# Optimization experiments

Measured on AMD Instinct MI355X. Metric: run time of the kernel, lower is better.

## Reference

```python
import jax, jax.numpy as jnp
import numpy as np
from jax import lax

D_FEAT, SEQ_LEN, D_MODEL, N_HEAD, N_LAYERS, D_FF, BATCH = 20, 20, 512, 8, 3, 2048, 4096


def _pe(L, D):
    pos = jnp.arange(L, dtype=jnp.float32)[:, None]
    div = jnp.exp(jnp.arange(0, D, 2, dtype=jnp.float32) * (-np.log(10000.0) / D))
    pe = jnp.zeros((L, D), dtype=jnp.float32)
    pe = pe.at[:, 0::2].set(jnp.sin(pos * div)).at[:, 1::2].set(jnp.cos(pos * div))
    return pe


def _ln(x, g, b, eps=1e-5):
    m = x.mean(-1, keepdims=True)
    v = ((x - m) ** 2).mean(-1, keepdims=True)
    return (x - m) * lax.rsqrt(v + eps) * g + b


def _circ_conv(x, w):
    # x [B,C,L]: Conv1d(C->1, k=3, circular padding=1, no bias) -> [B,L]
    xs = jnp.stack([jnp.roll(x, 1, -1), x, jnp.roll(x, -1, -1)], -1)  # [B,C,L,3]
    return jnp.einsum('bclk,ck->bl', xs, w)


def _projector(x, stats, wconv, W0, b0, W1, b1, W2):
    y = _circ_conv(x, wconv)                       # [B, d_feat]
    z = jnp.concatenate([y, stats[:, 0, :]], -1)   # [B, 2*d_feat]
    h = jax.nn.relu(z @ W0.T + b0)
    h = jax.nn.relu(h @ W1.T + b1)
    return h @ W2.T                                # no bias on last layer


def setup_inputs():
    key = jax.random.key(0)
    ks = iter(jax.random.split(key, 64))
    nrm = lambda shape, s=0.02: jax.random.normal(next(ks), shape, dtype=jnp.float32) * s
    zeros = lambda shape: jnp.zeros(shape, jnp.float32)
    ones = lambda shape: jnp.ones(shape, jnp.float32)
    return {
        'src': jax.random.normal(next(ks), (BATCH, SEQ_LEN, D_FEAT), dtype=jnp.float32),
        'W_feat': nrm((D_MODEL, D_FEAT)), 'b_feat': zeros((D_MODEL,)),
        'tau_conv': nrm((SEQ_LEN, 3), 0.1),
        'tau_W0': nrm((D_MODEL, 2 * D_FEAT)), 'tau_b0': zeros((D_MODEL,)),
        'tau_W1': nrm((D_MODEL, D_MODEL)), 'tau_b1': zeros((D_MODEL,)),
        'tau_W2': nrm((1, D_MODEL)),
        'del_conv': nrm((SEQ_LEN, 3), 0.1),
        'del_W0': nrm((D_MODEL, 2 * D_FEAT)), 'del_b0': zeros((D_MODEL,)),
        'del_W1': nrm((D_MODEL, D_MODEL)), 'del_b1': zeros((D_MODEL,)),
        'del_W2': nrm((SEQ_LEN, D_MODEL)),
        'Wq': nrm((N_LAYERS, D_MODEL, D_MODEL)), 'bq': zeros((N_LAYERS, D_MODEL)),
        'Wk': nrm((N_LAYERS, D_MODEL, D_MODEL)), 'bk': zeros((N_LAYERS, D_MODEL)),
        'Wv': nrm((N_LAYERS, D_MODEL, D_MODEL)), 'bv': zeros((N_LAYERS, D_MODEL)),
        'Wo': nrm((N_LAYERS, D_MODEL, D_MODEL)), 'bo': zeros((N_LAYERS, D_MODEL)),
        'Wc1': nrm((N_LAYERS, D_FF, D_MODEL)), 'bc1': zeros((N_LAYERS, D_FF)),
        'Wc2': nrm((N_LAYERS, D_MODEL, D_FF)), 'bc2': zeros((N_LAYERS, D_MODEL)),
        'ln1_g': ones((N_LAYERS, D_MODEL)), 'ln1_b': zeros((N_LAYERS, D_MODEL)),
        'ln2_g': ones((N_LAYERS, D_MODEL)), 'ln2_b': zeros((N_LAYERS, D_MODEL)),
        'lnf_g': ones((D_MODEL,)), 'lnf_b': zeros((D_MODEL,)),
        'W_pre': nrm((SEQ_LEN, D_MODEL)), 'b_pre': zeros((SEQ_LEN,)),
        'W_dec': nrm((1, SEQ_LEN)), 'b_dec': zeros((1,)),
    }


def reference(src, W_feat, b_feat, tau_conv, tau_W0, tau_b0, tau_W1, tau_b1, tau_W2,
              del_conv, del_W0, del_b0, del_W1, del_b1, del_W2,
              Wq, bq, Wk, bk, Wv, bv, Wo, bo, Wc1, bc1, Wc2, bc2,
              ln1_g, ln1_b, ln2_g, ln2_b, lnf_g, lnf_b, W_pre, b_pre, W_dec, b_dec):
    B, L, F = src.shape
    H = N_HEAD
    x_raw = lax.stop_gradient(src)
    mean_src = lax.stop_gradient(jnp.mean(src, axis=1, keepdims=True))        # [B,1,F]
    s = src - mean_src
    std_src = lax.stop_gradient(jnp.sqrt(jnp.var(s, axis=1, keepdims=True) + 1e-5))
    s = s / std_src
    tau = jnp.exp(_projector(x_raw, std_src, tau_conv, tau_W0, tau_b0, tau_W1, tau_b1, tau_W2))  # [B,1]
    delta = _projector(x_raw, mean_src, del_conv, del_W0, del_b0, del_W1, del_b1, del_W2)        # [B,L]
    x = s @ W_feat.T + b_feat + _pe(L, W_feat.shape[0])[None]                 # [B,L,D]
    dh = x.shape[-1] // H
    scale = np.float32(1.0 / np.sqrt(dh))
    for i in range(Wq.shape[0]):
        q = (x @ Wq[i].T + bq[i]).reshape(B, L, H, dh)
        k = (x @ Wk[i].T + bk[i]).reshape(B, L, H, dh)
        v = (x @ Wv[i].T + bv[i]).reshape(B, L, H, dh)
        # DSAttention: tau-rescaled, delta-shifted scores
        scores = jnp.einsum('blhe,bshe->bhls', q, k) * tau[:, :, None, None] + delta[:, None, None, :]
        A = jax.nn.softmax(scale * scores, axis=-1)
        o = jnp.einsum('bhls,bshd->blhd', A, v).reshape(B, L, -1)
        x = x + (o @ Wo[i].T + bo[i])
        x = _ln(x, ln1_g[i], ln1_b[i])
        y = jax.nn.relu(x @ Wc1[i].T + bc1[i])        # conv1d k=1 == linear
        y = y @ Wc2[i].T + bc2[i]
        x = _ln(x + y, ln2_g[i], ln2_b[i])
    x = _ln(x, lnf_g, lnf_b)
    out = (x @ W_pre.T + b_pre) * std_src + mean_src  # [B,L,L] (d_feat == seq_len)
    out = out[:, -1, :] @ W_dec.T + b_dec             # [B,1]
    return out[:, 0]
```

## Files before the change

### kernel.cpp

```cpp
#include <hip/hip_runtime.h>
#include <math.h>
#include <stdint.h>

#define BB 4096
#define LL 20
#define FE 20
#define DD 512
#define HH 8
#define DHD 64
#define FFD 2048
#define NLAY 3

typedef __bf16 bf16x8 __attribute__((ext_vector_type(8)));
typedef float f32x4 __attribute__((ext_vector_type(4)));

__device__ __forceinline__ void gload_lds16(const unsigned short* g, unsigned short* l){
  __builtin_amdgcn_global_load_lds(
      (const __attribute__((address_space(1))) void*)g,
      (__attribute__((address_space(3))) void*)l, 16, 0, 0);
}

__device__ __forceinline__ float wsum(float v){
#pragma unroll
  for (int o = 32; o > 0; o >>= 1) v += __shfl_xor(v, o, 64);
  return v;
}

__device__ __forceinline__ unsigned short f2b(float f){
  unsigned u = __float_as_uint(f);
  u += 0x7FFFu + ((u >> 16) & 1u);
  return (unsigned short)(u >> 16);
}
__device__ __forceinline__ float b2f(unsigned short b){
  return __uint_as_float(((unsigned)b) << 16);
}

__device__ __forceinline__ int2 xcd_swz(){
  const int nx = gridDim.x;
  const int nwg = nx * gridDim.y;
  const int orig = blockIdx.y * nx + blockIdx.x;
  const int q = nwg >> 3, r = nwg & 7;
  const int xcd = orig & 7, idx = orig >> 3;
  const int wg = (xcd < r ? xcd*(q+1) : r*(q+1) + (xcd-r)*q) + idx;
  return make_int2(wg % nx, wg / nx);
}

template<bool RELU, bool BIAS, bool RES>
__global__ __launch_bounds__(256) void bgemm(
    const unsigned short* __restrict__ A, int lda,
    const unsigned short* __restrict__ W, int ldw,
    const float* __restrict__ bias,
    const unsigned short* res, int ldr,
    unsigned short* __restrict__ Cout, int ldc, int K)
{
  __shared__ __align__(16) unsigned short Asm[2][128*32];
  __shared__ __align__(16) unsigned short Bsm[2][128*32];
  const int2 swz = xcd_swz();
  const int bn = swz.x << 7, bm = swz.y << 7;
  const int tid = threadIdx.x;
  const int wave = tid >> 6, lane = tid & 63;
  const int wr = wave >> 1, wc = wave & 1;
  const int sr = lane >> 2, slot = lane & 3;
  const int rg = lane & 15, cg = lane >> 4;

  f32x4 acc[4][4];
#pragma unroll
  for (int i = 0; i < 4; ++i)
#pragma unroll
    for (int j = 0; j < 4; ++j) acc[i][j] = (f32x4){0.f,0.f,0.f,0.f};

  auto stage = [&](int kt, int b){
    const int k0 = kt << 5;
#pragma unroll
    for (int i = 0; i < 2; ++i) {
      const int r  = (i<<6) + (wave<<4) + sr;
      const int ch = slot ^ ((r>>1)&3);
      gload_lds16(A + (size_t)(bm + r)*lda + k0 + (ch<<3),
                  &Asm[b][((i<<6) + (wave<<4))*32]);
      gload_lds16(W + (size_t)(bn + r)*ldw + k0 + (ch<<3),
                  &Bsm[b][((i<<6) + (wave<<4))*32]);
    }
  };

  auto compute = [&](int b){
    bf16x8 af[4], bfr[4];
#pragma unroll
    for (int mi = 0; mi < 4; ++mi){
      int r = (wr<<6) + (mi<<4) + rg;
      af[mi] = *(const bf16x8*)&Asm[b][r*32 + ((cg ^ ((r>>1)&3))<<3)];
    }
#pragma unroll
    for (int ni = 0; ni < 4; ++ni){
      int r = (wc<<6) + (ni<<4) + rg;
      bfr[ni] = *(const bf16x8*)&Bsm[b][r*32 + ((cg ^ ((r>>1)&3))<<3)];
    }
#pragma unroll
    for (int mi = 0; mi < 4; ++mi)
#pragma unroll
      for (int ni = 0; ni < 4; ++ni)
        acc[mi][ni] = __builtin_amdgcn_mfma_f32_16x16x32_bf16(af[mi], bfr[ni], acc[mi][ni], 0, 0, 0);
  };

  const int nt = K >> 5;
  stage(0, 0);
  __syncthreads();
  int cur = 0;
  for (int t = 0; t < nt; ++t){
    if (t + 1 < nt) stage(t + 1, cur ^ 1);
    compute(cur);
    __syncthreads();
    cur ^= 1;
  }

#pragma unroll
  for (int mi = 0; mi < 4; ++mi){
#pragma unroll
    for (int ni = 0; ni < 4; ++ni){
      const int row0 = bm + (wr<<6) + (mi<<4) + (cg<<2);
      const int col  = bn + (wc<<6) + (ni<<4) + rg;
      float bv = BIAS ? bias[col] : 0.f;
#pragma unroll
      for (int j = 0; j < 4; ++j){
        float v = acc[mi][ni][j] + bv;
        if (RES)  v += b2f(res[(size_t)(row0+j)*ldr + col]);
        if (RELU) v = fmaxf(v, 0.f);
        Cout[(size_t)(row0+j)*ldc + col] = f2b(v);
      }
    }
  }
}

template<bool RELU, bool BIAS, bool RES>
__global__ __launch_bounds__(256) void bgemm64(
    const unsigned short* __restrict__ A, int lda,
    const unsigned short* __restrict__ W, int ldw,
    const float* __restrict__ bias,
    const unsigned short* res, int ldr,
    unsigned short* __restrict__ Cout, int ldc, int K)
{
  __shared__ __align__(16) unsigned short Asm[2][64*32];
  __shared__ __align__(16) unsigned short Bsm[2][128*32];
  const int2 swz = xcd_swz();
  const int bn = swz.x << 7, bm = swz.y << 6;
  const int tid = threadIdx.x;
  const int wave = tid >> 6, lane = tid & 63;
  const int sr = lane >> 2, slot = lane & 3;
  const int rg = lane & 15, cg = lane >> 4;

  f32x4 acc[4][2];
#pragma unroll
  for (int i = 0; i < 4; ++i)
#pragma unroll
    for (int j = 0; j < 2; ++j) acc[i][j] = (f32x4){0.f,0.f,0.f,0.f};

  auto stage = [&](int kt, int b){
    const int k0 = kt << 5;
    {
      const int r  = (wave<<4) + sr;
      const int ch = slot ^ ((r>>1)&3);
      gload_lds16(A + (size_t)(bm + r)*lda + k0 + (ch<<3),
                  &Asm[b][(wave<<4)*32]);
    }
#pragma unroll
    for (int i = 0; i < 2; ++i) {
      const int r  = (i<<6) + (wave<<4) + sr;
      const int ch = slot ^ ((r>>1)&3);
      gload_lds16(W + (size_t)(bn + r)*ldw + k0 + (ch<<3),
                  &Bsm[b][((i<<6) + (wave<<4))*32]);
    }
  };

  auto compute = [&](int b){
    bf16x8 af[4], bfr[2];
#pragma unroll
    for (int mi = 0; mi < 4; ++mi){
      int r = (mi<<4) + rg;
      af[mi] = *(const bf16x8*)&Asm[b][r*32 + ((cg ^ ((r>>1)&3))<<3)];
    }
#pragma unroll
    for (int ni = 0; ni < 2; ++ni){
      int r = (wave<<5) + (ni<<4) + rg;
      bfr[ni] = *(const bf16x8*)&Bsm[b][r*32 + ((cg ^ ((r>>1)&3))<<3)];
    }
#pragma unroll
    for (int mi = 0; mi < 4; ++mi)
#pragma unroll
      for (int ni = 0; ni < 2; ++ni)
        acc[mi][ni] = __builtin_amdgcn_mfma_f32_16x16x32_bf16(af[mi], bfr[ni], acc[mi][ni], 0, 0, 0);
  };

  const int nt = K >> 5;
  stage(0, 0);
  __syncthreads();
  int cur = 0;
  for (int t = 0; t < nt; ++t){
    if (t + 1 < nt) stage(t + 1, cur ^ 1);
    compute(cur);
    __syncthreads();
    cur ^= 1;
  }

#pragma unroll
  for (int mi = 0; mi < 4; ++mi){
#pragma unroll
    for (int ni = 0; ni < 2; ++ni){
      const int row0 = bm + (mi<<4) + (cg<<2);
      const int col  = bn + (wave<<5) + (ni<<4) + rg;
      float bv = BIAS ? bias[col] : 0.f;
#pragma unroll
      for (int j = 0; j < 4; ++j){
        float v = acc[mi][ni][j] + bv;
        if (RES)  v += b2f(res[(size_t)(row0+j)*ldr + col]);
        if (RELU) v = fmaxf(v, 0.f);
        Cout[(size_t)(row0+j)*ldc + col] = f2b(v);
      }
    }
  }
}

template<bool RELU, bool BIAS, bool PE>
__global__ __launch_bounds__(256) void gemm_xwt(
    const float* __restrict__ A, int lda,
    const float* __restrict__ W, int ldw,
    const float* __restrict__ bias,
    float* __restrict__ C, int ldc,
    int M, int N, int K,
    const float* __restrict__ pe, unsigned short* __restrict__ xbout)
{
  __shared__ float As[16][72];
  __shared__ float Ws[16][72];
  const int bm = blockIdx.y << 6, bn = blockIdx.x << 6;
  const int tid = threadIdx.x;
  const int tx = tid & 15, ty = tid >> 4;
  const int lr = tid >> 2;
  const int lc = (tid & 3) << 2;
  float acc[4][4] = {{0.f}};
  const float* Ap = A + (size_t)(bm + lr) * lda;
  const float* Wp = W + (size_t)(bn + lr) * ldw;
  for (int k0 = 0; k0 < K; k0 += 16) {
    float4 av, wv;
    if (k0 + 16 <= K) {
      av = *(const float4*)(Ap + k0 + lc);
      wv = *(const float4*)(Wp + k0 + lc);
    } else {
      float aa[4] = {0,0,0,0}, ww[4] = {0,0,0,0};
#pragma unroll
      for (int j = 0; j < 4; ++j){ int kk = k0 + lc + j; if (kk < K){ aa[j] = Ap[kk]; ww[j] = Wp[kk]; } }
      av = make_float4(aa[0],aa[1],aa[2],aa[3]);
      wv = make_float4(ww[0],ww[1],ww[2],ww[3]);
    }
    As[lc+0][lr]=av.x; As[lc+1][lr]=av.y; As[lc+2][lr]=av.z; As[lc+3][lr]=av.w;
    Ws[lc+0][lr]=wv.x; Ws[lc+1][lr]=wv.y; Ws[lc+2][lr]=wv.z; Ws[lc+3][lr]=wv.w;
    __syncthreads();
#pragma unroll
    for (int k = 0; k < 16; ++k) {
      const float4 a = *(const float4*)(&As[k][ty<<2]);
      const float4 b = *(const float4*)(&Ws[k][tx<<2]);
      acc[0][0]+=a.x*b.x; acc[0][1]+=a.x*b.y; acc[0][2]+=a.x*b.z; acc[0][3]+=a.x*b.w;
      acc[1][0]+=a.y*b.x; acc[1][1]+=a.y*b.y; acc[1][2]+=a.y*b.z; acc[1][3]+=a.y*b.w;
      acc[2][0]+=a.z*b.x; acc[2][1]+=a.z*b.y; acc[2][2]+=a.z*b.z; acc[2][3]+=a.z*b.w;
      acc[3][0]+=a.w*b.x; acc[3][1]+=a.w*b.y; acc[3][2]+=a.w*b.z; acc[3][3]+=a.w*b.w;
    }
    __syncthreads();
  }
#pragma unroll
  for (int i = 0; i < 4; ++i) {
    const int m = bm + (ty<<2) + i;
#pragma unroll
    for (int j = 0; j < 4; ++j) {
      const int col = bn + (tx<<2) + j;
      float v = acc[i][j];
      if (BIAS) v += bias[col];
      if (PE)   v += pe[(m % LL)*DD + col];
      if (RELU) v = fmaxf(v, 0.f);
      if (PE) xbout[(size_t)m*ldc + col] = f2b(v);
      else    C[(size_t)m*ldc + col] = v;
    }
  }
}

__global__ void cvt_bf16_kernel(const float* __restrict__ in, unsigned short* __restrict__ out, int n){
  int i = blockIdx.x * 256 + threadIdx.x;
  if (i < n) out[i] = f2b(in[i]);
}

__global__ void concat_bias_kernel(const float* __restrict__ bq, const float* __restrict__ bk,
                                   const float* __restrict__ bv, float* __restrict__ bqkv){
  int i = blockIdx.x * 256 + threadIdx.x;
  if (i >= NLAY*1536) return;
  int l = i / 1536, r = i % 1536;
  int s = r >> 9, j = r & 511;
  const float* srcp = (s == 0) ? bq : (s == 1) ? bk : bv;
  bqkv[i] = srcp[l*DD + j];
}

__global__ void pe_kernel(float* __restrict__ pe){
  int i = blockIdx.x * 256 + threadIdx.x;
  int l = i >> 8, hd = i & 255;
  float dv = expf((2.f * hd) * (-9.210340371976184f / 512.f));
  float a = (float)l * dv;
  pe[l*DD + 2*hd]     = sinf(a);
  pe[l*DD + 2*hd + 1] = cosf(a);
}

__global__ void stats_kernel(const float* __restrict__ src, float* __restrict__ mean,
                             float* __restrict__ stdv, int nbf){
  int i = blockIdx.x * 256 + threadIdx.x;
  if (i >= nbf) return;
  int b = i / FE, f = i % FE;
  const float* p = src + (size_t)b * (LL*FE) + f;
  float v[LL]; float s = 0.f;
#pragma unroll
  for (int l = 0; l < LL; ++l){ v[l] = p[l*FE]; s += v[l]; }
  float m = s * (1.f/LL);
  float q = 0.f;
#pragma unroll
  for (int l = 0; l < LL; ++l){ float d = v[l]-m; q += d*d; }
  mean[i] = m;
  stdv[i] = sqrtf(q * (1.f/LL) + 1e-5f);
}

__global__ void snorm_kernel(const float* __restrict__ src, const float* __restrict__ mean,
                             const float* __restrict__ stdv, float* __restrict__ s, int n){
  int i = blockIdx.x * 256 + threadIdx.x;
  if (i >= n) return;
  int b = i / (LL*FE);
  int f = i % FE;
  int bf = b*FE + f;
  s[i] = (src[i] - mean[bf]) / stdv[bf];
}

__global__ __launch_bounds__(64) void convz_kernel(
    const float* __restrict__ src, const float* __restrict__ wt, const float* __restrict__ wd,
    const float* __restrict__ mean, const float* __restrict__ stdv,
    float* __restrict__ z_tau, float* __restrict__ z_del)
{
  int b = blockIdx.x;
  __shared__ float ss[LL*FE];
  __shared__ float wct[LL*3], wcd[LL*3];
  for (int idx = threadIdx.x; idx < LL*FE; idx += 64) ss[idx] = src[(size_t)b*LL*FE + idx];
  if (threadIdx.x < 60){ wct[threadIdx.x] = wt[threadIdx.x]; wcd[threadIdx.x] = wd[threadIdx.x]; }
  __syncthreads();
  if (threadIdx.x < 40) {
    int f = threadIdx.x % FE;
    bool isdel = threadIdx.x >= FE;
    const float* w = isdel ? wcd : wct;
    int fm = (f + FE - 1) % FE, fp = (f + 1) % FE;
    float acc = 0.f;
#pragma unroll
    for (int t = 0; t < LL; ++t){
      const float* r = ss + t*FE;
      acc += r[fm]*w[t*3+0] + r[f]*w[t*3+1] + r[fp]*w[t*3+2];
    }
    if (isdel){ z_del[b*40 + f] = acc; z_del[b*40 + 20 + f] = mean[b*FE + f]; }
    else      { z_tau[b*40 + f] = acc; z_tau[b*40 + 20 + f] = stdv[b*FE + f]; }
  }
}

__global__ __launch_bounds__(256) void tau_head(const float* __restrict__ h, const float* __restrict__ W2, float* __restrict__ tau){
  const int b = (blockIdx.x << 2) + (threadIdx.x >> 6);
  const int lane = threadIdx.x & 63;
  const float* hb = h + (size_t)b * DD;
  float s = 0.f;
#pragma unroll
  for (int j = 0; j < 8; ++j){ int d0 = lane + j*64; s += hb[d0]*W2[d0]; }
  s = wsum(s);
  if (lane == 0) tau[b] = expf(s);
}

__global__ __launch_bounds__(256) void delta_head(const float* __restrict__ h, const float* __restrict__ W2, float* __restrict__ delta){
  const int b = blockIdx.x;
  const int w = threadIdx.x >> 6, lane = threadIdx.x & 63;
  const float* hb = h + (size_t)b * DD;
  for (int f = w; f < FE; f += 4){
    float s = 0.f;
#pragma unroll
    for (int j = 0; j < 8; ++j){ int d0 = lane + j*64; s += hb[d0]*W2[(size_t)f*DD + d0]; }
    s = wsum(s);
    if (lane == 0) delta[b*FE + f] = s;
  }
}

__global__ __launch_bounds__(256) void attn_kernel(
    unsigned short* __restrict__ qkv,
    const float* __restrict__ tau, const float* __restrict__ delta)
{
  const int bh = blockIdx.x;
  const int b = bh >> 3, h = bh & 7;
  __shared__ float qs[LL][68];
  __shared__ float kt[DHD][25];
  __shared__ float vs[LL][DHD];
  __shared__ float ps[LL][LL+1];
  const size_t base = (size_t)b * LL * 1536 + h * DHD;
  unsigned short* qg = qkv + base;
  const unsigned short* kg = qkv + base + 512;
  const unsigned short* vg = qkv + base + 1024;

  for (int it = threadIdx.x; it < LL*16; it += 256) {
    const int l = it >> 4, c = it & 15;
    const ushort4 qv = *(const ushort4*)(qg + l*1536 + c*4);
    const ushort4 kv = *(const ushort4*)(kg + l*1536 + c*4);
    const ushort4 vv = *(const ushort4*)(vg + l*1536 + c*4);
    qs[l][c*4+0]=b2f(qv.x); qs[l][c*4+1]=b2f(qv.y); qs[l][c*4+2]=b2f(qv.z); qs[l][c*4+3]=b2f(qv.w);
    kt[c*4+0][l]=b2f(kv.x); kt[c*4+1][l]=b2f(kv.y); kt[c*4+2][l]=b2f(kv.z); kt[c*4+3][l]=b2f(kv.w);
    vs[l][c*4+0]=b2f(vv.x); vs[l][c*4+1]=b2f(vv.y); vs[l][c*4+2]=b2f(vv.z); vs[l][c*4+3]=b2f(vv.w);
  }
  __syncthreads();

  const float ta = tau[b];
  for (int idx = threadIdx.x; idx < LL*LL; idx += 256) {
    const int l = idx / LL, s2 = idx % LL;
    float d = 0.f;
#pragma unroll
    for (int e = 0; e < DHD; ++e) d += qs[l][e]*kt[e][s2];
    ps[l][s2] = 0.125f * (d * ta + delta[b*FE + s2]);
  }
  __syncthreads();

  if (threadIdx.x < LL) {
    const int l = threadIdx.x;
    float m = -1e30f;
#pragma unroll
    for (int s2 = 0; s2 < LL; ++s2) m = fmaxf(m, ps[l][s2]);
    float sum = 0.f;
#pragma unroll
    for (int s2 = 0; s2 < LL; ++s2){ float e2 = expf(ps[l][s2]-m); ps[l][s2] = e2; sum += e2; }
    const float r = 1.f / sum;
#pragma unroll
    for (int s2 = 0; s2 < LL; ++s2) ps[l][s2] *= r;
  }
  __syncthreads();

  for (int it = threadIdx.x; it < LL*16; it += 256) {
    const int l = it >> 4, c = it & 15;
    float4 o = {0.f,0.f,0.f,0.f};
#pragma unroll
    for (int s2 = 0; s2 < LL; ++s2) {
      const float p = ps[l][s2];
      const float4 vv = *(const float4*)&vs[s2][c*4];
      o.x += p*vv.x; o.y += p*vv.y; o.z += p*vv.z; o.w += p*vv.w;
    }
    ushort4 ov;
    ov.x = f2b(o.x); ov.y = f2b(o.y); ov.z = f2b(o.z); ov.w = f2b(o.w);
    *(ushort4*)(qg + l*1536 + c*4) = ov;
  }
}

__global__ __launch_bounds__(64) void attn19_kernel(
    const unsigned short* __restrict__ kvb, const unsigned short* __restrict__ q19,
    unsigned short* __restrict__ o19,
    const float* __restrict__ tau, const float* __restrict__ delta)
{
  const int bh = blockIdx.x;
  const int b = bh >> 3, h = bh & 7;
  __shared__ float ks[LL][DHD], vs[LL][DHD];
  const unsigned short* kg = kvb + (size_t)b * LL * 1024 + h * DHD;
  const unsigned short* vg = kg + 512;
  for (int it = threadIdx.x; it < LL*16; it += 64) {
    const int l = it >> 4, c = it & 15;
    const ushort4 kv = *(const ushort4*)(kg + l*1024 + c*4);
    const ushort4 vv = *(const ushort4*)(vg + l*1024 + c*4);
    ks[l][c*4+0]=b2f(kv.x); ks[l][c*4+1]=b2f(kv.y); ks[l][c*4+2]=b2f(kv.z); ks[l][c*4+3]=b2f(kv.w);
    vs[l][c*4+0]=b2f(vv.x); vs[l][c*4+1]=b2f(vv.y); vs[l][c*4+2]=b2f(vv.z); vs[l][c*4+3]=b2f(vv.w);
  }
  __syncthreads();
  const int e = threadIdx.x;
  const float q = b2f(q19[(size_t)b*DD + h*DHD + e]);
  const float ta = tau[b];
  float p[LL];
  float m = -1e30f;
#pragma unroll
  for (int s2 = 0; s2 < LL; ++s2){
    float d = q * ks[s2][e];
    d = wsum(d);
    p[s2] = 0.125f * (d * ta + delta[b*FE + s2]);
    m = fmaxf(m, p[s2]);
  }
  float sum = 0.f;
#pragma unroll
  for (int s2 = 0; s2 < LL; ++s2){ p[s2] = expf(p[s2]-m); sum += p[s2]; }
  const float r = 1.f / sum;
  float o = 0.f;
#pragma unroll
  for (int s2 = 0; s2 < LL; ++s2) o += p[s2] * vs[s2][e];
  o19[(size_t)b*DD + h*DHD + e] = f2b(o * r);
}

__global__ __launch_bounds__(256) void ln_bf16_kernel(
    unsigned short* __restrict__ x, const float* __restrict__ g, const float* __restrict__ be)
{
  const int row = (blockIdx.x << 2) + (threadIdx.x >> 6);
  const int lane = threadIdx.x & 63;
  const int d0 = lane * 8;
  unsigned short* xr = x + (size_t)row * DD + d0;
  const ushort4 a = *(const ushort4*)xr;
  const ushort4 b = *(const ushort4*)(xr + 4);
  float v[8];
  v[0]=b2f(a.x); v[1]=b2f(a.y); v[2]=b2f(a.z); v[3]=b2f(a.w);
  v[4]=b2f(b.x); v[5]=b2f(b.y); v[6]=b2f(b.z); v[7]=b2f(b.w);
  float s = v[0]+v[1]+v[2]+v[3]+v[4]+v[5]+v[6]+v[7];
  s = wsum(s);
  const float mu = s * (1.f/DD);
  float q = 0.f;
#pragma unroll
  for (int j = 0; j < 8; ++j){ float d = v[j]-mu; q += d*d; }
  q = wsum(q);
  const float rcp = rsqrtf(q*(1.f/DD) + 1e-5f);
  const float4 g0 = *(const float4*)(g + d0), g1 = *(const float4*)(g + d0 + 4);
  const float4 b0 = *(const float4*)(be + d0), b1 = *(const float4*)(be + d0 + 4);
  ushort4 u0, u1;
  u0.x = f2b((v[0]-mu)*rcp*g0.x + b0.x); u0.y = f2b((v[1]-mu)*rcp*g0.y + b0.y);
  u0.z = f2b((v[2]-mu)*rcp*g0.z + b0.z); u0.w = f2b((v[3]-mu)*rcp*g0.w + b0.w);
  u1.x = f2b((v[4]-mu)*rcp*g1.x + b1.x); u1.y = f2b((v[5]-mu)*rcp*g1.y + b1.y);
  u1.z = f2b((v[6]-mu)*rcp*g1.z + b1.z); u1.w = f2b((v[7]-mu)*rcp*g1.w + b1.w);
  *(ushort4*)xr = u0; *(ushort4*)(xr + 4) = u1;
}

__global__ __launch_bounds__(64) void final_kernel(
    const unsigned short* __restrict__ x19,
    const float* __restrict__ g, const float* __restrict__ be,
    const float* __restrict__ W_pre, const float* __restrict__ b_pre,
    const float* __restrict__ mean, const float* __restrict__ stdv,
    const float* __restrict__ W_dec, const float* __restrict__ b_dec,
    float* __restrict__ out)
{
  const int b = blockIdx.x;
  const int lane = threadIdx.x;
  const unsigned short* xr = x19 + (size_t)b * DD;
  float vals[8];
  float s = 0.f;
#pragma unroll
  for (int j = 0; j < 8; ++j){ vals[j] = b2f(xr[lane + j*64]); s += vals[j]; }
  s = wsum(s);
  const float mu = s * (1.f/DD);
  float vs = 0.f;
#pragma unroll
  for (int j = 0; j < 8; ++j){ float d = vals[j]-mu; vs += d*d; }
  vs = wsum(vs);
  const float rs = rsqrtf(vs*(1.f/DD) + 1e-5f);
#pragma unroll
  for (int j = 0; j < 8; ++j){ int d0 = lane + j*64; vals[j] = (vals[j]-mu)*rs*g[d0] + be[d0]; }
  float accb = 0.f;
  for (int f = 0; f < FE; ++f){
    float d = 0.f;
#pragma unroll
    for (int j = 0; j < 8; ++j){ int d0 = lane + j*64; d += vals[j]*W_pre[f*DD + d0]; }
    d = wsum(d);
    float o = (d + b_pre[f]) * stdv[b*FE + f] + mean[b*FE + f];
    accb += o * W_dec[f];
  }
  if (lane == 0) out[b] = accb + b_dec[0];
}

extern "C" void kernel_launch(void* const* d_in, const int* in_sizes, int n_in,
                              void* d_out, int out_size, void* d_ws, size_t ws_size,
                              hipStream_t stream) {
  const float* src     = (const float*)d_in[0];
  const float* W_feat  = (const float*)d_in[1];
  const float* b_feat  = (const float*)d_in[2];
  const float* tau_conv= (const float*)d_in[3];
  const float* tau_W0  = (const float*)d_in[4];
  const float* tau_b0  = (const float*)d_in[5];
  const float* tau_W1  = (const float*)d_in[6];
  const float* tau_b1  = (const float*)d_in[7];
  const float* tau_W2  = (const float*)d_in[8];
  const float* del_conv= (const float*)d_in[9];
  const float* del_W0  = (const float*)d_in[10];
  const float* del_b0  = (const float*)d_in[11];
  const float* del_W1  = (const float*)d_in[12];
  const float* del_b1  = (const float*)d_in[13];
  const float* del_W2  = (const float*)d_in[14];
  const float* Wq = (const float*)d_in[15]; const float* bq = (const float*)d_in[16];
  const float* Wk = (const float*)d_in[17]; const float* bk = (const float*)d_in[18];
  const float* Wv = (const float*)d_in[19]; const float* bv = (const float*)d_in[20];
  const float* Wo = (const float*)d_in[21]; const float* bo = (const float*)d_in[22];
  const float* Wc1= (const float*)d_in[23]; const float* bc1= (const float*)d_in[24];
  const float* Wc2= (const float*)d_in[25]; const float* bc2= (const float*)d_in[26];
  const float* ln1_g=(const float*)d_in[27]; const float* ln1_b=(const float*)d_in[28];
  const float* ln2_g=(const float*)d_in[29]; const float* ln2_b=(const float*)d_in[30];
  const float* lnf_g=(const float*)d_in[31]; const float* lnf_b=(const float*)d_in[32];
  const float* W_pre=(const float*)d_in[33]; const float* b_pre=(const float*)d_in[34];
  const float* W_dec=(const float*)d_in[35]; const float* b_dec=(const float*)d_in[36];
  float* out = (float*)d_out;

  auto need_floats = [](size_t cb)->size_t{
    size_t fl = 10240 + 2*(size_t)BB*FE;
    fl += 4718592 + 4608;
    fl += 2*(size_t)BB*40;
    fl += 2*(size_t)BB*DD;
    fl += BB + (size_t)BB*FE;
    fl += cb*25600;
    fl += 64*64;
    return fl;
  };
  size_t maxCB = BB;
  while (maxCB > 64 && need_floats(maxCB)*4 > ws_size) maxCB -= 64;
  size_t nch = (BB + maxCB - 1) / maxCB;
  size_t CB = ((BB + nch - 1) / nch + 63) & ~(size_t)63;
  if (CB > maxCB) CB = maxCB;

  float* w = (float*)d_ws;
  size_t off = 0;
  auto take = [&](size_t n){ float* p = w + off; off += (n + 63) & ~(size_t)63; return p; };
  float* pe    = take(LL*DD);
  float* meanG = take((size_t)BB*FE);
  float* stdvG = take((size_t)BB*FE);
  unsigned short* Wqkvb = (unsigned short*)take((size_t)NLAY*1536*DD/2);
  unsigned short* Wob   = (unsigned short*)take((size_t)NLAY*DD*DD/2);
  unsigned short* Wc1b  = (unsigned short*)take((size_t)NLAY*FFD*DD/2);
  unsigned short* Wc2b  = (unsigned short*)take((size_t)NLAY*DD*FFD/2);
  float* bqkv  = take(NLAY*1536);
  float* z_tau = take((size_t)BB*40);
  float* z_del = take((size_t)BB*40);
  float* h_a   = take((size_t)BB*DD);
  float* h_b   = take((size_t)BB*DD);
  float* taubG = take(BB);
  float* deltaG= take((size_t)BB*FE);
  unsigned short* xb = (unsigned short*)take(CB*LL*DD/2);
  float* unionBuf = take(CB*20480);
  float* sbuf = unionBuf;
  unsigned short* qkvb = (unsigned short*)unionBuf;
  unsigned short* hb   = (unsigned short*)unionBuf;
  unsigned short* kvb  = (unsigned short*)unionBuf;
  unsigned short* q19b = (unsigned short*)(unionBuf + CB*10240);
  unsigned short* o19b = (unsigned short*)(unionBuf + CB*10496);
  unsigned short* hb19 = (unsigned short*)(unionBuf + CB*10752);
  unsigned short* x19b = (unsigned short*)(unionBuf + CB*11776);

  pe_kernel<<<20, 256, 0, stream>>>(pe);
  stats_kernel<<<(BB*FE + 255)/256, 256, 0, stream>>>(src, meanG, stdvG, BB*FE);
  {
    const int nqkv = DD*DD;
    for (int l = 0; l < NLAY; ++l) {
      cvt_bf16_kernel<<<(nqkv+255)/256, 256, 0, stream>>>(Wq + (size_t)l*nqkv, Wqkvb + (size_t)l*1536*DD, nqkv);
      cvt_bf16_kernel<<<(nqkv+255)/256, 256, 0, stream>>>(Wk + (size_t)l*nqkv, Wqkvb + (size_t)l*1536*DD + (size_t)512*DD, nqkv);
      cvt_bf16_kernel<<<(nqkv+255)/256, 256, 0, stream>>>(Wv + (size_t)l*nqkv, Wqkvb + (size_t)l*1536*DD + (size_t)1024*DD, nqkv);
    }
    int n1 = NLAY*DD*DD, n2 = NLAY*FFD*DD;
    cvt_bf16_kernel<<<(n1+255)/256, 256, 0, stream>>>(Wo, Wob, n1);
    cvt_bf16_kernel<<<(n2+255)/256, 256, 0, stream>>>(Wc1, Wc1b, n2);
    cvt_bf16_kernel<<<(n2+255)/256, 256, 0, stream>>>(Wc2, Wc2b, n2);
    concat_bias_kernel<<<(NLAY*1536+255)/256, 256, 0, stream>>>(bq, bk, bv, bqkv);
  }
  {
    const dim3 gP(8, BB/64);
    convz_kernel<<<BB, 64, 0, stream>>>(src, tau_conv, del_conv, meanG, stdvG, z_tau, z_del);
    gemm_xwt<true,true,false><<<gP, 256, 0, stream>>>(z_tau,40, tau_W0,40, tau_b0, h_a,DD, BB,DD,40, nullptr,nullptr);
    gemm_xwt<true,true,false><<<gP, 256, 0, stream>>>(h_a,DD, tau_W1,DD, tau_b1, h_b,DD, BB,DD,DD, nullptr,nullptr);
    tau_head<<<BB/4, 256, 0, stream>>>(h_b, tau_W2, taubG);
    gemm_xwt<true,true,false><<<gP, 256, 0, stream>>>(z_del,40, del_W0,40, del_b0, h_a,DD, BB,DD,40, nullptr,nullptr);
    gemm_xwt<true,true,false><<<gP, 256, 0, stream>>>(h_a,DD, del_W1,DD, del_b1, h_b,DD, BB,DD,DD, nullptr,nullptr);
    delta_head<<<BB, 256, 0, stream>>>(h_b, del_W2, deltaG);
  }

  const int iL = NLAY - 1;

  for (size_t b0 = 0; b0 < BB; b0 += CB) {
    const size_t cb = (BB - b0 < CB) ? (BB - b0) : CB;
    const int cm = (int)(cb * LL);
    const float* srcC  = src + b0*LL*FE;
    const float* meanC = meanG + b0*FE;
    const float* stdvC = stdvG + b0*FE;
    const float* taub  = taubG + b0;
    const float* delta = deltaG + b0*FE;

    const dim3 gEmb(8, cm/64);
    const dim3 gQKV(1536/128, cm/128);
    const dim3 gD(DD/128, cm/128);
    const dim3 gF1(FFD/128, cm/128);
    const dim3 gKV(1024/128, cm/128);
    const dim3 g19D(DD/128, (int)cb/64);
    const dim3 g19F(FFD/128, (int)cb/64);

    snorm_kernel<<<(int)((cb*LL*FE + 255)/256), 256, 0, stream>>>(srcC, meanC, stdvC, sbuf, (int)(cb*LL*FE));
    gemm_xwt<false,true,true><<<gEmb, 256, 0, stream>>>(sbuf,FE, W_feat,FE, b_feat, nullptr,DD, cm,DD,FE, pe, xb);

    for (int i = 0; i < iL; ++i) {
      const size_t wOfs = (size_t)i * DD * DD;
      const size_t fOfs = (size_t)i * FFD * DD;
      bgemm<false,true,false><<<gQKV, 256, 0, stream>>>(xb,DD, Wqkvb + (size_t)i*1536*DD,DD, bqkv + i*1536, nullptr,0, qkvb,1536, DD);
      attn_kernel<<<(int)cb*HH, 256, 0, stream>>>(qkvb, taub, delta);
      bgemm<false,true,true><<<gD, 256, 0, stream>>>(qkvb,1536, Wob+wOfs,DD, bo+i*DD, xb,DD, xb,DD, DD);
      ln_bf16_kernel<<<cm/4, 256, 0, stream>>>(xb, ln1_g+i*DD, ln1_b+i*DD);
      bgemm<true,true,false><<<gF1, 256, 0, stream>>>(xb,DD, Wc1b+fOfs,DD, bc1+i*FFD, nullptr,0, hb,FFD, DD);
      bgemm<false,true,true><<<gD, 256, 0, stream>>>(hb,FFD, Wc2b+fOfs,FFD, bc2+i*DD, xb,DD, xb,DD, FFD);
      ln_bf16_kernel<<<cm/4, 256, 0, stream>>>(xb, ln2_g+i*DD, ln2_b+i*DD);
    }

    {
      const size_t wOfs = (size_t)iL * DD * DD;
      const size_t fOfs = (size_t)iL * FFD * DD;
      bgemm<false,true,false><<<gKV, 256, 0, stream>>>(xb,DD, Wqkvb + (size_t)iL*1536*DD + (size_t)512*DD,DD, bqkv + iL*1536 + 512, nullptr,0, kvb,1024, DD);
      bgemm64<false,true,false><<<g19D, 256, 0, stream>>>(xb + 19*DD, LL*DD, Wqkvb + (size_t)iL*1536*DD,DD, bqkv + iL*1536, nullptr,0, q19b,DD, DD);
      attn19_kernel<<<(int)cb*HH, 64, 0, stream>>>(kvb, q19b, o19b, taub, delta);
      bgemm64<false,true,true><<<g19D, 256, 0, stream>>>(o19b,DD, Wob+wOfs,DD, bo+iL*DD, xb + 19*DD, LL*DD, x19b,DD, DD);
      ln_bf16_kernel<<<(int)cb/4, 256, 0, stream>>>(x19b, ln1_g+iL*DD, ln1_b+iL*DD);
      bgemm64<true,true,false><<<g19F, 256, 0, stream>>>(x19b,DD, Wc1b+fOfs,DD, bc1+iL*FFD, nullptr,0, hb19,FFD, DD);
      bgemm64<false,true,true><<<g19D, 256, 0, stream>>>(hb19,FFD, Wc2b+fOfs,FFD, bc2+iL*DD, x19b,DD, x19b,DD, FFD);
      ln_bf16_kernel<<<(int)cb/4, 256, 0, stream>>>(x19b, ln2_g+iL*DD, ln2_b+iL*DD);
    }

    final_kernel<<<(int)cb, 64, 0, stream>>>(x19b, lnf_g, lnf_b, W_pre, b_pre, meanC, stdvC, W_dec, b_dec, out + b0);
  }
}
```

Measured before the change: 2.519 ms.

## Deepen bgemm LDS pipeline to four stages with explicit vmcnt waits

Changes the bf16 GEMM main loop from double-buffered to four-buffer LDS staging, prefetching three K-tiles ahead. It waits on vmcnt(8) instead of a full sync and issues the next loads right after the LDS fragment reads. It also raises wave priority around the MFMA block to overlap global loads with compute. LDS use doubles to 64KB per block, which may lower occupancy. Near the end of K the loop re-stages the last tile, adding redundant loads.

Result: slower. 2.621 ms (+4.0%).

```diff
diff --git a/kernel.cpp b/kernel.cpp
--- a/kernel.cpp
+++ b/kernel.cpp
@@ -53,8 +53,8 @@
     const unsigned short* res, int ldr,
     unsigned short* __restrict__ Cout, int ldc, int K)
 {
-  __shared__ __align__(16) unsigned short Asm[2][128*32];
-  __shared__ __align__(16) unsigned short Bsm[2][128*32];
+  __shared__ __align__(16) unsigned short Asm[4][128*32];
+  __shared__ __align__(16) unsigned short Bsm[4][128*32];
   const int2 swz = xcd_swz();
   const int bn = swz.x << 7, bm = swz.y << 7;
   const int tid = threadIdx.x;
@@ -69,7 +69,7 @@
 #pragma unroll
     for (int j = 0; j < 4; ++j) acc[i][j] = (f32x4){0.f,0.f,0.f,0.f};
 
-  auto stage = [&](int kt, int b){
+  auto stageA = [&](int kt, int b){
     const int k0 = kt << 5;
 #pragma unroll
     for (int i = 0; i < 2; ++i) {
@@ -77,39 +77,59 @@
       const int ch = slot ^ ((r>>1)&3);
       gload_lds16(A + (size_t)(bm + r)*lda + k0 + (ch<<3),
                   &Asm[b][((i<<6) + (wave<<4))*32]);
+    }
+  };
+  auto stageB = [&](int kt, int b){
+    const int k0 = kt << 5;
+#pragma unroll
+    for (int i = 0; i < 2; ++i) {
+      const int r  = (i<<6) + (wave<<4) + sr;
+      const int ch = slot ^ ((r>>1)&3);
       gload_lds16(W + (size_t)(bn + r)*ldw + k0 + (ch<<3),
                   &Bsm[b][((i<<6) + (wave<<4))*32]);
     }
   };
 
-  auto compute = [&](int b){
+  const int nt = K >> 5;
+  stageA(0, 0); stageB(0, 0);
+  stageA(1, 1); stageB(1, 1);
+  stageA(2, 2); stageB(2, 2);
+
+  for (int t = 0; t < nt; ++t){
+    asm volatile("s_waitcnt vmcnt(8)" ::: "memory");
+    __builtin_amdgcn_s_barrier();
+    __builtin_amdgcn_sched_barrier(0);
+    asm volatile("" ::: "memory");
+
+    const int cb = t & 3;
+    const int ts = (t + 3 < nt) ? t + 3 : nt - 1;
+    const int sb = (t + 3) & 3;
+
     bf16x8 af[4], bfr[4];
 #pragma unroll
     for (int mi = 0; mi < 4; ++mi){
       int r = (wr<<6) + (mi<<4) + rg;
-      af[mi] = *(const bf16x8*)&Asm[b][r*32 + ((cg ^ ((r>>1)&3))<<3)];
+      af[mi] = *(const bf16x8*)&Asm[cb][r*32 + ((cg ^ ((r>>1)&3))<<3)];
     }
 #pragma unroll
     for (int ni = 0; ni < 4; ++ni){
       int r = (wc<<6) + (ni<<4) + rg;
-      bfr[ni] = *(const bf16x8*)&Bsm[b][r*32 + ((cg ^ ((r>>1)&3))<<3)];
-    }
+      bfr[ni] = *(const bf16x8*)&Bsm[cb][r*32 + ((cg ^ ((r>>1)&3))<<3)];
+    }
+    stageA(ts, sb);
+    stageB(ts, sb);
+
+    __builtin_amdgcn_s_setprio(1);
 #pragma unroll
     for (int mi = 0; mi < 4; ++mi)
 #pragma unroll
       for (int ni = 0; ni < 4; ++ni)
         acc[mi][ni] = __builtin_amdgcn_mfma_f32_16x16x32_bf16(af[mi], bfr[ni], acc[mi][ni], 0, 0, 0);
-  };
-
-  const int nt = K >> 5;
-  stage(0, 0);
-  __syncthreads();
-  int cur = 0;
-  for (int t = 0; t < nt; ++t){
-    if (t + 1 < nt) stage(t + 1, cur ^ 1);
-    compute(cur);
-    __syncthreads();
-    cur ^= 1;
+    __builtin_amdgcn_s_setprio(0);
+
+    asm volatile("" ::: "memory");
+    __builtin_amdgcn_sched_barrier(0);
+    __builtin_amdgcn_s_barrier();
   }
 
 #pragma unroll
```
